# Kernel optimization log

Measured on AMD Instinct MI355X. Metric: run time of the kernel, lower is better.

Reference implementation:

```python
import jax, jax.numpy as jnp
import numpy as np

B, S, D, H = 2, 2048, 768, 12
DK = D // H


def setup_inputs() -> dict:
    key = jax.random.key(0)
    ks = jax.random.split(key, 11)
    sc = 1.0 / np.sqrt(D)
    return {
        "q": jax.random.normal(ks[0], (B, S, D), jnp.float32),
        "k": jax.random.normal(ks[1], (B, S, D), jnp.float32),
        "v": jax.random.normal(ks[2], (B, S, D), jnp.float32),
        "Wq": jax.random.normal(ks[3], (D, D), jnp.float32) * sc,
        "bq": jnp.zeros((D,), jnp.float32),
        "Wk": jax.random.normal(ks[4], (D, D), jnp.float32) * sc,
        "bk": jnp.zeros((D,), jnp.float32),
        "Wv": jax.random.normal(ks[5], (D, D), jnp.float32) * sc,
        "bv": jnp.zeros((D,), jnp.float32),
        "Wc": jax.random.normal(ks[6], (D, D), jnp.float32) * sc,
        "bc": jnp.zeros((D,), jnp.float32),
    }


def _split(t):
    # Faithful to source: view(B, n_head, S, d_k) WITHOUT transpose —
    # heads partition the flattened (S*D) buffer, not the feature axis.
    return t.reshape(B, H, S, DK)


def reference(q, k, v, Wq, bq, Wk, bk, Wv, bv, Wc, bc):
    q = _split(q @ Wq.T + bq)  # [B,H,S,DK]
    k = _split(k @ Wk.T + bk)
    v = _split(v @ Wv.T + bv)
    score = jnp.einsum("bhqd,bhkd->bhqk", q, k) / np.sqrt(DK)  # [B,H,S,S]
    attn = jax.nn.softmax(score, axis=-1)
    # Faithful bug in source: uses pre-softmax score, not attn.
    out = jnp.einsum("bhqk,bhkd->bhqd", score, v)  # [B,H,S,DK]
    out = out.transpose(0, 2, 1, 3).reshape(B, S, D)  # concat
    out = out @ Wc.T + bc
    return out, attn
```

## Files before the change

### kernel.cpp

```cpp
#include <hip/hip_runtime.h>
#include <hip/hip_bf16.h>


#define S_LEN   2048
#define D_MODEL 768
#define NHEAD   12
#define DKH     64
#define BSROWS  4096
#define HEADSZ  (S_LEN * DKH)
#define WELEMS  (D_MODEL * D_MODEL)

typedef __attribute__((ext_vector_type(4))) float f32x4;
typedef __attribute__((ext_vector_type(8))) short s16x8;

static __device__ __forceinline__ unsigned cvtpk(float lo, float hi) {
    unsigned r;
    asm("v_cvt_pk_bf16_f32 %0, %1, %2" : "=v"(r) : "v"(lo), "v"(hi));
    return r;
}

static __device__ __forceinline__ short f2bf(float f) {
    return (short)cvtpk(f, f);
}

static __device__ __forceinline__ s16x8 cvt8(f32x4 a, f32x4 b) {
    union { unsigned u[4]; s16x8 v; } o;
    o.u[0] = cvtpk(a[0], a[1]);
    o.u[1] = cvtpk(a[2], a[3]);
    o.u[2] = cvtpk(b[0], b[1]);
    o.u[3] = cvtpk(b[2], b[3]);
    return o.v;
}

static __device__ __forceinline__ void gload16(const void* g, void* l) {
    __builtin_amdgcn_global_load_lds((const __attribute__((address_space(1))) void*)g,
                                     (__attribute__((address_space(3))) void*)l, 16, 0, 0);
}

static __device__ __forceinline__ s16x8 ldfrag(const short* tile, int row, int c16) {
    int byte = row * 128 + ((c16 * 16) ^ ((row & 7) << 4));
    return *(const s16x8*)((const char*)tile + byte);
}

__global__ __launch_bounds__(256) void prep_w(const float* __restrict__ W0,
                                              const float* __restrict__ W1,
                                              const float* __restrict__ W2,
                                              const float* __restrict__ W3,
                                              short* __restrict__ dst)
{
    const float* src = (blockIdx.y == 0) ? W0 : (blockIdx.y == 1) ? W1
                     : (blockIdx.y == 2) ? W2 : W3;
    short* d = dst + (size_t)blockIdx.y * WELEMS;
    int i = (blockIdx.x * 256 + threadIdx.x) * 8;
    f32x4 a = *(const f32x4*)(src + i);
    f32x4 b = *(const f32x4*)(src + i + 4);
    *(s16x8*)(d + i) = cvt8(a, b);
}

template<int A_F32, int OUT_F32>
static __device__ __forceinline__ void gemm_body128(const void* __restrict__ Av,
                                                    const short* __restrict__ Wb,
                                                    const float* __restrict__ bias,
                                                    void* __restrict__ Cv,
                                                    int mt, int nt)
{
    __shared__ short As[8192];
    __shared__ short Bs[8192];
    const int t = threadIdx.x, w = t >> 6, lane = t & 63;
    const int lrow = lane & 15, lgrp = lane >> 4;
    const int wr = w >> 1, wc = w & 1;

    f32x4 acc[4][4];
#pragma unroll
    for (int m = 0; m < 4; ++m)
#pragma unroll
        for (int n = 0; n < 4; ++n) acc[m][n] = {0.f, 0.f, 0.f, 0.f};

    for (int kk = 0; kk < 768; kk += 64) {
        __syncthreads();
#pragma unroll
        for (int j = 0; j < 4; ++j) {
            int cid = t + j * 256, row = cid >> 3, ch = cid & 7;
            gload16(Wb + (size_t)(nt * 128 + row) * 768 + kk + ((ch ^ (row & 7)) * 8),
                    (char*)Bs + j * 4096 + w * 1024);
        }
        if (A_F32) {
#pragma unroll
            for (int j = 0; j < 2; ++j) {
                int cid = t + j * 256, row = cid >> 2, q4 = cid & 3;
                const float* src = (const float*)Av + (size_t)(mt * 128 + row) * 768 + kk + q4 * 16;
                f32x4 v0 = *(const f32x4*)(src);
                f32x4 v1 = *(const f32x4*)(src + 4);
                f32x4 v2 = *(const f32x4*)(src + 8);
                f32x4 v3 = *(const f32x4*)(src + 12);
                int c0 = q4 * 2;
                *(s16x8*)((char*)As + row * 128 + (((c0    ) ^ (row & 7)) * 16)) = cvt8(v0, v1);
                *(s16x8*)((char*)As + row * 128 + (((c0 + 1) ^ (row & 7)) * 16)) = cvt8(v2, v3);
            }
        } else {
#pragma unroll
            for (int j = 0; j < 4; ++j) {
                int cid = t + j * 256, row = cid >> 3, ch = cid & 7;
                gload16((const short*)Av + (size_t)(mt * 128 + row) * 768 + kk + ((ch ^ (row & 7)) * 8),
                        (char*)As + j * 4096 + w * 1024);
            }
        }
        __syncthreads();
#pragma unroll
        for (int kc = 0; kc < 2; ++kc) {
            s16x8 af[4], bfr[4];
#pragma unroll
            for (int m = 0; m < 4; ++m) af[m] = ldfrag(As, wr * 64 + m * 16 + lrow, kc * 4 + lgrp);
#pragma unroll
            for (int n = 0; n < 4; ++n) bfr[n] = ldfrag(Bs, wc * 64 + n * 16 + lrow, kc * 4 + lgrp);
            __builtin_amdgcn_s_setprio(1);
#pragma unroll
            for (int m = 0; m < 4; ++m)
#pragma unroll
                for (int n = 0; n < 4; ++n)
                    acc[m][n] = __builtin_amdgcn_mfma_f32_16x16x32_bf16(af[m], bfr[n], acc[m][n], 0, 0, 0);
            __builtin_amdgcn_s_setprio(0);
        }
    }
#pragma unroll
    for (int n = 0; n < 4; ++n) {
        int col = nt * 128 + wc * 64 + n * 16 + lrow;
        float bvv = bias[col];
#pragma unroll
        for (int m = 0; m < 4; ++m)
#pragma unroll
            for (int r = 0; r < 4; ++r) {
                int row = mt * 128 + wr * 64 + m * 16 + lgrp * 4 + r;
                float v = acc[m][n][r] + bvv;
                if (OUT_F32) ((float*)Cv)[(size_t)row * 768 + col] = v;
                else         ((short*)Cv)[(size_t)row * 768 + col] = f2bf(v);
            }
    }
}

template<int OUT_F32>
static __device__ __forceinline__ void gemm_body64(const short* __restrict__ Av,
                                                   const short* __restrict__ Wb,
                                                   const float* __restrict__ bias,
                                                   void* __restrict__ Cv,
                                                   int mt, int nt)
{
    __shared__ short As[4096];
    __shared__ short Bs[4096];
    const int t = threadIdx.x, w = t >> 6, lane = t & 63;
    const int lrow = lane & 15, lgrp = lane >> 4;
    const int wr = w >> 1, wc = w & 1;

    f32x4 acc[2][2];
#pragma unroll
    for (int m = 0; m < 2; ++m)
#pragma unroll
        for (int n = 0; n < 2; ++n) acc[m][n] = {0.f, 0.f, 0.f, 0.f};

    for (int kk = 0; kk < 768; kk += 64) {
        __syncthreads();
#pragma unroll
        for (int j = 0; j < 2; ++j) {
            int cid = t + j * 256, row = cid >> 3, ch = cid & 7;
            int cs = (ch ^ (row & 7)) * 8;
            gload16(Av + (size_t)(mt * 64 + row) * 768 + kk + cs,
                    As + w * 512 + j * 2048);
            gload16(Wb + (size_t)(nt * 64 + row) * 768 + kk + cs,
                    Bs + w * 512 + j * 2048);
        }
        __syncthreads();
#pragma unroll
        for (int kc = 0; kc < 2; ++kc) {
            s16x8 af[2], bfr[2];
#pragma unroll
            for (int m = 0; m < 2; ++m) af[m] = ldfrag(As, wr * 32 + m * 16 + lrow, kc * 4 + lgrp);
#pragma unroll
            for (int n = 0; n < 2; ++n) bfr[n] = ldfrag(Bs, wc * 32 + n * 16 + lrow, kc * 4 + lgrp);
            __builtin_amdgcn_s_setprio(1);
#pragma unroll
            for (int m = 0; m < 2; ++m)
#pragma unroll
                for (int n = 0; n < 2; ++n)
                    acc[m][n] = __builtin_amdgcn_mfma_f32_16x16x32_bf16(af[m], bfr[n], acc[m][n], 0, 0, 0);
            __builtin_amdgcn_s_setprio(0);
        }
    }
#pragma unroll
    for (int n = 0; n < 2; ++n) {
        int col = nt * 64 + wc * 32 + n * 16 + lrow;
        float bvv = bias[col];
#pragma unroll
        for (int m = 0; m < 2; ++m)
#pragma unroll
            for (int r = 0; r < 4; ++r) {
                int row = mt * 64 + wr * 32 + m * 16 + lgrp * 4 + r;
                float v = acc[m][n][r] + bvv;
                if (OUT_F32) ((float*)Cv)[(size_t)row * 768 + col] = v;
                else         ((short*)Cv)[(size_t)row * 768 + col] = f2bf(v);
            }
    }
}

__global__ __launch_bounds__(256) void gemm_qkv(const float* __restrict__ q,
                                                const float* __restrict__ k,
                                                const float* __restrict__ v,
                                                const short* __restrict__ Wbf,
                                                const float* __restrict__ bq,
                                                const float* __restrict__ bk,
                                                const float* __restrict__ bv,
                                                short* __restrict__ Qw,
                                                short* __restrict__ Kw,
                                                short* __restrict__ Vw)
{
    const int bid = blockIdx.x;
    const int idx = bid >> 3;
    const int panel = (bid & 7) * 12 + idx / 6;
    const int nt = idx % 6;
    const int z = panel / 32, mt = panel % 32;
    const float* A; const float* bias; short* C;
    if (z == 0)      { A = q; bias = bq; C = Qw; }
    else if (z == 1) { A = k; bias = bk; C = Kw; }
    else             { A = v; bias = bv; C = Vw; }
    gemm_body128<1, 0>(A, Wbf + (size_t)z * WELEMS, bias, C, mt, nt);
}

__global__ __launch_bounds__(256) void gemm_out(const short* __restrict__ Ob,
                                                const short* __restrict__ Wcb,
                                                const float* __restrict__ bc,
                                                float* __restrict__ out)
{
    const int bid = blockIdx.x;
    const int idx = (bid & 7) * 96 + (bid >> 3);
    const int mt = idx / 12, nt = idx % 12;
    gemm_body64<1>(Ob, Wcb, bc, out, mt, nt);
}

__global__ __launch_bounds__(256) void vtrans(const short* __restrict__ Vw,
                                              short* __restrict__ Vt)
{
    const int sblk = blockIdx.x, bh = blockIdx.y;
    const short* src = Vw + (size_t)bh * HEADSZ;
    short* dst = Vt + (size_t)bh * HEADSZ;
    const int t = threadIdx.x;
#pragma unroll
    for (int j = 0; j < 2; ++j) {
        int cid = t + j * 256, dk = cid >> 3, ch = cid & 7;
        int s0 = sblk * 64 + ch * 8;
        s16x8 vv;
#pragma unroll
        for (int e = 0; e < 8; ++e) vv[e] = src[(size_t)(s0 + e) * DKH + dk];
        *(s16x8*)(dst + (size_t)dk * S_LEN + s0) = vv;
    }
}

__global__ __launch_bounds__(256, 4) void attn_fused2(const short* __restrict__ Qb,
                                                      const short* __restrict__ Kb,
                                                      const short* __restrict__ Vtb,
                                                      short* __restrict__ Ob,
                                                      float* __restrict__ attn)
{
    __shared__ short lds[20480];
    short* Qs = lds;
    const float CE = 0.18033688f;

    const int bid = blockIdx.x;
    const int swz = (bid & 7) * 96 + (bid >> 3);
    const int qb = swz & 31, bh = swz >> 5;
    const int t = threadIdx.x, w = t >> 6, lane = t & 63;
    const int lrow = lane & 15, lgrp = lane >> 4;
    const int b = bh / NHEAD, h = bh % NHEAD;
    const short* Qh = Qb + (size_t)bh * HEADSZ;
    const short* Kh = Kb + (size_t)bh * HEADSZ;
    const short* Vth = Vtb + (size_t)bh * HEADSZ;
    const int q0 = qb * 64;

#define STAGE_K4(dst, kt) do {                                                  \
    _Pragma("unroll")                                                           \
    for (int j = 0; j < 2; ++j) {                                               \
        int cid = t + j * 256, row = cid >> 3, ch = cid & 7;                    \
        gload16(Kh + (size_t)((kt) * 64 + row) * DKH + ((ch ^ (row & 7)) * 8),  \
                (dst) + w * 512 + j * 2048);                                    \
    } } while (0)

#define STAGE_V4(dst, kt) do {                                                  \
    _Pragma("unroll")                                                           \
    for (int j = 0; j < 2; ++j) {                                               \
        int cid = t + j * 256, row = cid >> 3, ch = cid & 7;                    \
        gload16(Vth + (size_t)row * S_LEN + (kt) * 64 + ((ch ^ (row & 7)) * 8), \
                (dst) + w * 512 + j * 2048);                                    \
    } } while (0)

#pragma unroll
    for (int j = 0; j < 2; ++j) {
        int cid = t + j * 256, row = cid >> 3, ch = cid & 7;
        gload16(Qh + (size_t)(q0 + row) * DKH + ((ch ^ (row & 7)) * 8),
                Qs + w * 512 + j * 2048);
    }
    STAGE_K4(lds + 4096, 0);
    STAGE_V4(lds + 12288, 0);
    __syncthreads();

    s16x8 aq[2];
#pragma unroll
    for (int c = 0; c < 2; ++c)
        aq[c] = ldfrag(Qs, w * 16 + lrow, c * 4 + lgrp);
    __syncthreads();

    f32x4 pv[4];
#pragma unroll
    for (int n = 0; n < 4; ++n) pv[n] = {0.f, 0.f, 0.f, 0.f};
    float zp[4] = {0.f, 0.f, 0.f, 0.f};

    short* SW = lds + w * 1024;
    int cur = 0;

    for (int kt = 0; kt < 32; ++kt) {
        if (kt) __syncthreads();
        if (kt < 31) {
            STAGE_K4(lds + 4096 + (cur ^ 1) * 4096, kt + 1);
            STAGE_V4(lds + 12288 + (cur ^ 1) * 4096, kt + 1);
        }
        const short* Kc = lds + 4096 + cur * 4096;
        const short* Vc = lds + 12288 + cur * 4096;

#pragma unroll
        for (int n = 0; n < 4; ++n) {
            f32x4 s = {0.f, 0.f, 0.f, 0.f};
            __builtin_amdgcn_s_setprio(1);
#pragma unroll
            for (int c = 0; c < 2; ++c) {
                s16x8 bk = ldfrag(Kc, n * 16 + lrow, c * 4 + lgrp);
                s = __builtin_amdgcn_mfma_f32_16x16x32_bf16(aq[c], bk, s, 0, 0, 0);
            }
            __builtin_amdgcn_s_setprio(0);
            int kcol2 = (n * 16 + lrow) * 2;
#pragma unroll
            for (int r = 0; r < 4; ++r) {
                zp[r] += exp2f(s[r] * CE);
                int qa = lgrp * 4 + r;
                *(short*)((char*)SW + qa * 128 + (kcol2 ^ ((qa & 7) << 4)))
                    = f2bf(s[r] * 0.125f);
            }
        }
        s16x8 as[2];
#pragma unroll
        for (int c = 0; c < 2; ++c)
            as[c] = ldfrag(SW, lrow, c * 4 + lgrp);
        __builtin_amdgcn_s_setprio(1);
#pragma unroll
        for (int n = 0; n < 4; ++n) {
#pragma unroll
            for (int c = 0; c < 2; ++c) {
                s16x8 bv = ldfrag(Vc, n * 16 + lrow, c * 4 + lgrp);
                pv[n] = __builtin_amdgcn_mfma_f32_16x16x32_bf16(as[c], bv, pv[n], 0, 0, 0);
            }
        }
        __builtin_amdgcn_s_setprio(0);
        cur ^= 1;
    }

    float* fvz = (float*)SW;
#pragma unroll
    for (int r = 0; r < 4; ++r) {
        float z = zp[r];
        z += __shfl_xor(z, 1, 16);
        z += __shfl_xor(z, 2, 16);
        z += __shfl_xor(z, 4, 16);
        z += __shfl_xor(z, 8, 16);
        if (lrow == 0)
            fvz[lgrp * 4 + r] = 1.0f / z;
    }
    __syncthreads();

    STAGE_K4(lds + 4096, 0);
    STAGE_K4(lds + 8192, 1);

#pragma unroll
    for (int n = 0; n < 4; ++n)
#pragma unroll
        for (int r = 0; r < 4; ++r) {
            int srow = q0 + w * 16 + lgrp * 4 + r;
            Ob[((size_t)b * S_LEN + srow) * D_MODEL + h * DKH + n * 16 + lrow]
                = f2bf(pv[n][r]);
        }

    float l2invz = __log2f(fvz[lrow]);

    float* aw = attn + (size_t)bh * S_LEN * S_LEN;
    for (int kt2 = 0; kt2 < 32; kt2 += 2) {
        __syncthreads();
        if (kt2 + 2 < 32) {
            STAGE_K4(lds + 4096 + ((kt2 + 2) & 3) * 4096, kt2 + 2);
            STAGE_K4(lds + 4096 + ((kt2 + 3) & 3) * 4096, kt2 + 3);
        }
#pragma unroll
        for (int u = 0; u < 2; ++u) {
            const int kt = kt2 + u;
            const short* Kc = lds + 4096 + (kt & 3) * 4096;
#pragma unroll
            for (int n = 0; n < 4; ++n) {
                f32x4 s = {0.f, 0.f, 0.f, 0.f};
                __builtin_amdgcn_s_setprio(1);
#pragma unroll
                for (int c = 0; c < 2; ++c) {
                    s16x8 bk = ldfrag(Kc, n * 16 + lrow, c * 4 + lgrp);
                    s = __builtin_amdgcn_mfma_f32_16x16x32_bf16(bk, aq[c], s, 0, 0, 0);
                }
                __builtin_amdgcn_s_setprio(0);
                f32x4 a0;
#pragma unroll
                for (int r = 0; r < 4; ++r)
                    a0[r] = exp2f(fmaf(s[r], CE, l2invz));
                int kbase = kt * 64 + n * 16 + lgrp * 4;
                *(f32x4*)(aw + (size_t)(q0 + w * 16 + lrow) * S_LEN + kbase) = a0;
            }
        }
    }
#undef STAGE_K4
#undef STAGE_V4
}

extern "C" void kernel_launch(void* const* d_in, const int* in_sizes, int n_in,
                              void* d_out, int out_size, void* d_ws, size_t ws_size,
                              hipStream_t stream)
{
    const float* q  = (const float*)d_in[0];
    const float* k  = (const float*)d_in[1];
    const float* v  = (const float*)d_in[2];
    const float* Wq = (const float*)d_in[3];
    const float* bq = (const float*)d_in[4];
    const float* Wk = (const float*)d_in[5];
    const float* bk = (const float*)d_in[6];
    const float* Wv = (const float*)d_in[7];
    const float* bv = (const float*)d_in[8];
    const float* Wc = (const float*)d_in[9];
    const float* bc = (const float*)d_in[10];

    float* out  = (float*)d_out;
    float* attn = out + (size_t)BSROWS * D_MODEL;

    short* Wbf  = (short*)d_ws;
    short* Qw   = Wbf + (size_t)4 * WELEMS;
    short* Kw   = Qw + (size_t)BSROWS * D_MODEL;
    short* VwOb = Kw + (size_t)BSROWS * D_MODEL;
    short* Vt   = VwOb + (size_t)BSROWS * D_MODEL;

    prep_w<<<dim3(288, 4), dim3(256), 0, stream>>>(Wq, Wk, Wv, Wc, Wbf);

    gemm_qkv<<<dim3(576), dim3(256), 0, stream>>>(q, k, v, Wbf, bq, bk, bv,
                                                  Qw, Kw, VwOb);

    vtrans<<<dim3(32, 24), dim3(256), 0, stream>>>(VwOb, Vt);

    attn_fused2<<<dim3(768), dim3(256), 0, stream>>>(Qw, Kw, Vt, VwOb , attn);

    gemm_out<<<dim3(768), dim3(256), 0, stream>>>(VwOb , Wbf + (size_t)3 * WELEMS,
                                                  bc, out);
}
```

Before: 212.8 us.

## Split attention pass-1 into 2x2 query/key warp tiles with cross-warp reduction

Pass 1 now splits work so each wave computes a 32-query by 32-key score sub-tile instead of 16 queries by 64 keys. Each K fragment is reused across two query rows, and each V fragment is reused across two score fragments. Partial PV accumulators and row sums from the two key-half waves are combined through LDS after the loop, and waves with kh==0 write O. This reduces LDS fragment loads per MFMA but adds extra registers, an LDS reduction step, and a barrier.

```diff
diff --git a/kernel.cpp b/kernel.cpp
--- a/kernel.cpp
+++ b/kernel.cpp
@@ -268,6 +268,7 @@
     const int qb = swz & 31, bh = swz >> 5;
     const int t = threadIdx.x, w = t >> 6, lane = t & 63;
     const int lrow = lane & 15, lgrp = lane >> 4;
+    const int qh = w & 1, kh = w >> 1;
     const int b = bh / NHEAD, h = bh % NHEAD;
     const short* Qh = Qb + (size_t)bh * HEADSZ;
     const short* Kh = Kb + (size_t)bh * HEADSZ;
@@ -300,16 +301,23 @@
     STAGE_V4(lds + 12288, 0);
     __syncthreads();
 
-    s16x8 aq[2];
+    s16x8 aqA[2][2], aqB[2];
+#pragma unroll
+    for (int m = 0; m < 2; ++m)
+#pragma unroll
+        for (int c = 0; c < 2; ++c)
+            aqA[m][c] = ldfrag(Qs, qh * 32 + m * 16 + lrow, c * 4 + lgrp);
 #pragma unroll
     for (int c = 0; c < 2; ++c)
-        aq[c] = ldfrag(Qs, w * 16 + lrow, c * 4 + lgrp);
+        aqB[c] = ldfrag(Qs, w * 16 + lrow, c * 4 + lgrp);
     __syncthreads();
 
-    f32x4 pv[4];
-#pragma unroll
-    for (int n = 0; n < 4; ++n) pv[n] = {0.f, 0.f, 0.f, 0.f};
-    float zp[4] = {0.f, 0.f, 0.f, 0.f};
+    f32x4 pv[2][4];
+#pragma unroll
+    for (int m = 0; m < 2; ++m)
+#pragma unroll
+        for (int n = 0; n < 4; ++n) pv[m][n] = {0.f, 0.f, 0.f, 0.f};
+    float zp[2][4] = {{0.f,0.f,0.f,0.f},{0.f,0.f,0.f,0.f}};
 
     short* SW = lds + w * 1024;
     int cur = 0;
@@ -323,68 +331,100 @@
         const short* Kc = lds + 4096 + cur * 4096;
         const short* Vc = lds + 12288 + cur * 4096;
 
+        f32x4 s[2][2];
+#pragma unroll
+        for (int m = 0; m < 2; ++m)
+#pragma unroll
+            for (int n = 0; n < 2; ++n) s[m][n] = {0.f, 0.f, 0.f, 0.f};
+        __builtin_amdgcn_s_setprio(1);
+#pragma unroll
+        for (int n = 0; n < 2; ++n)
+#pragma unroll
+            for (int c = 0; c < 2; ++c) {
+                s16x8 bk = ldfrag(Kc, kh * 32 + n * 16 + lrow, c * 4 + lgrp);
+                s[0][n] = __builtin_amdgcn_mfma_f32_16x16x32_bf16(aqA[0][c], bk, s[0][n], 0, 0, 0);
+                s[1][n] = __builtin_amdgcn_mfma_f32_16x16x32_bf16(aqA[1][c], bk, s[1][n], 0, 0, 0);
+            }
+        __builtin_amdgcn_s_setprio(0);
+
+#pragma unroll
+        for (int m = 0; m < 2; ++m)
+#pragma unroll
+            for (int n = 0; n < 2; ++n) {
+#pragma unroll
+                for (int r = 0; r < 4; ++r) {
+                    zp[m][r] += exp2f(s[m][n][r] * CE);
+                    int qa = m * 16 + lgrp * 4 + r;
+                    *(short*)((char*)SW + qa * 64 +
+                              ((n * 32 + lrow * 2) ^ (((qa >> 2) & 3) << 4)))
+                        = f2bf(s[m][n][r] * 0.125f);
+                }
+            }
+
+        s16x8 asb[2];
+#pragma unroll
+        for (int m = 0; m < 2; ++m) {
+            int row = m * 16 + lrow;
+            asb[m] = *(const s16x8*)((char*)SW + row * 64 +
+                                     ((lgrp * 16) ^ ((((row >> 2) & 3)) << 4)));
+        }
+        __builtin_amdgcn_s_setprio(1);
 #pragma unroll
         for (int n = 0; n < 4; ++n) {
-            f32x4 s = {0.f, 0.f, 0.f, 0.f};
-            __builtin_amdgcn_s_setprio(1);
-#pragma unroll
-            for (int c = 0; c < 2; ++c) {
-                s16x8 bk = ldfrag(Kc, n * 16 + lrow, c * 4 + lgrp);
-                s = __builtin_amdgcn_mfma_f32_16x16x32_bf16(aq[c], bk, s, 0, 0, 0);
-            }
-            __builtin_amdgcn_s_setprio(0);
-            int kcol2 = (n * 16 + lrow) * 2;
-#pragma unroll
-            for (int r = 0; r < 4; ++r) {
-                zp[r] += exp2f(s[r] * CE);
-                int qa = lgrp * 4 + r;
-                *(short*)((char*)SW + qa * 128 + (kcol2 ^ ((qa & 7) << 4)))
-                    = f2bf(s[r] * 0.125f);
-            }
-        }
-        s16x8 as[2];
-#pragma unroll
-        for (int c = 0; c < 2; ++c)
-            as[c] = ldfrag(SW, lrow, c * 4 + lgrp);
-        __builtin_amdgcn_s_setprio(1);
-#pragma unroll
-        for (int n = 0; n < 4; ++n) {
-#pragma unroll
-            for (int c = 0; c < 2; ++c) {
-                s16x8 bv = ldfrag(Vc, n * 16 + lrow, c * 4 + lgrp);
-                pv[n] = __builtin_amdgcn_mfma_f32_16x16x32_bf16(as[c], bv, pv[n], 0, 0, 0);
-            }
+            s16x8 bv = ldfrag(Vc, n * 16 + lrow, kh * 4 + lgrp);
+            pv[0][n] = __builtin_amdgcn_mfma_f32_16x16x32_bf16(asb[0], bv, pv[0][n], 0, 0, 0);
+            pv[1][n] = __builtin_amdgcn_mfma_f32_16x16x32_bf16(asb[1], bv, pv[1][n], 0, 0, 0);
         }
         __builtin_amdgcn_s_setprio(0);
         cur ^= 1;
     }
-
-    float* fvz = (float*)SW;
-#pragma unroll
-    for (int r = 0; r < 4; ++r) {
-        float z = zp[r];
-        z += __shfl_xor(z, 1, 16);
-        z += __shfl_xor(z, 2, 16);
-        z += __shfl_xor(z, 4, 16);
-        z += __shfl_xor(z, 8, 16);
-        if (lrow == 0)
-            fvz[lgrp * 4 + r] = 1.0f / z;
+    __syncthreads();
+
+    float* fvz = (float*)lds;
+    float* pvx = (float*)(lds + 12288);
+#pragma unroll
+    for (int m = 0; m < 2; ++m)
+#pragma unroll
+        for (int r = 0; r < 4; ++r) {
+            float z = zp[m][r];
+            z += __shfl_xor(z, 1, 16);
+            z += __shfl_xor(z, 2, 16);
+            z += __shfl_xor(z, 4, 16);
+            z += __shfl_xor(z, 8, 16);
+            if (lrow == 0)
+                fvz[kh * 64 + qh * 32 + m * 16 + lgrp * 4 + r] = z;
+        }
+    if (kh == 1) {
+        float* dst = pvx + qh * 2048 + lane * 4;
+#pragma unroll
+        for (int m = 0; m < 2; ++m)
+#pragma unroll
+            for (int n = 0; n < 4; ++n)
+                *(f32x4*)(dst + (m * 4 + n) * 256) = pv[m][n];
     }
     __syncthreads();
 
     STAGE_K4(lds + 4096, 0);
     STAGE_K4(lds + 8192, 1);
 
-#pragma unroll
-    for (int n = 0; n < 4; ++n)
-#pragma unroll
-        for (int r = 0; r < 4; ++r) {
-            int srow = q0 + w * 16 + lgrp * 4 + r;
-            Ob[((size_t)b * S_LEN + srow) * D_MODEL + h * DKH + n * 16 + lrow]
-                = f2bf(pv[n][r]);
-        }
-
-    float l2invz = __log2f(fvz[lrow]);
+    if (kh == 0) {
+        const float* src = pvx + qh * 2048 + lane * 4;
+#pragma unroll
+        for (int m = 0; m < 2; ++m)
+#pragma unroll
+            for (int n = 0; n < 4; ++n) {
+                pv[m][n] += *(const f32x4*)(src + (m * 4 + n) * 256);
+#pragma unroll
+                for (int r = 0; r < 4; ++r) {
+                    int srow = q0 + qh * 32 + m * 16 + lgrp * 4 + r;
+                    Ob[((size_t)b * S_LEN + srow) * D_MODEL + h * DKH + n * 16 + lrow]
+                        = f2bf(pv[m][n][r]);
+                }
+            }
+    }
+
+    float ztot = fvz[w * 16 + lrow] + fvz[64 + w * 16 + lrow];
+    float l2invz = -__log2f(ztot);
 
     float* aw = attn + (size_t)bh * S_LEN * S_LEN;
     for (int kt2 = 0; kt2 < 32; kt2 += 2) {
@@ -404,7 +444,7 @@
 #pragma unroll
                 for (int c = 0; c < 2; ++c) {
                     s16x8 bk = ldfrag(Kc, n * 16 + lrow, c * 4 + lgrp);
-                    s = __builtin_amdgcn_mfma_f32_16x16x32_bf16(bk, aq[c], s, 0, 0, 0);
+                    s = __builtin_amdgcn_mfma_f32_16x16x32_bf16(bk, aqB[c], s, 0, 0, 0);
                 }
                 __builtin_amdgcn_s_setprio(0);
                 f32x4 a0;
```

Result: no change. 209.3 us (-1.6%).
